# Kernel tuning notes

Hardware: AMD Instinct MI355X
Metric: run time of the kernel (lower is better)

The kernel has to match this reference:

```python
import jax, jax.numpy as jnp
import numpy as np

H = 16          # nhead
N_LAYERS = 4    # stacks (weights are SHARED across stacks, as in the torch module)
PAD_IDX = 1
EPS = 1e-6
NEG = -1e9


def _pos_encoding(S, d):
    den = jnp.exp(-jnp.arange(0, d, 2, dtype=jnp.float32) * (np.log(10000.0) / d))
    ang = jnp.arange(S, dtype=jnp.float32)[:, None] * den[None, :]  # (S, d/2)
    pe = jnp.zeros((S, d), jnp.float32)
    pe = pe.at[:, 0::2].set(jnp.sin(ang)).at[:, 1::2].set(jnp.cos(ang))
    return pe


def _layer_norm(x, g, b):
    mu = jnp.mean(x, axis=-1, keepdims=True)
    var = jnp.mean((x - mu) ** 2, axis=-1, keepdims=True)
    return (x - mu) * jax.lax.rsqrt(var + EPS) * g + b


def _split_heads(x):
    B, S, d = x.shape
    return x.reshape(B, S, H, d // H).transpose(0, 2, 1, 3)  # (B,H,S,dk)


def _mha(q_in, k_in, v_in, mask, wq, bq, wk, bk, wv, bv, wo, bo):
    q = _split_heads(q_in @ wq + bq)
    k = _split_heads(k_in @ wk + bk)
    v = _split_heads(v_in @ wv + bv)
    dk = v.shape[-1]
    score = jnp.einsum('bhqd,bhkd->bhqk', q, k) / jnp.sqrt(jnp.float32(dk))
    if mask is not None:
        score = jnp.where(mask, score, NEG)
    p = jax.nn.softmax(score, axis=-1)
    out = jnp.einsum('bhqk,bhkd->bhqd', p, v)
    B, _, S, _ = out.shape
    out = out.transpose(0, 2, 1, 3).reshape(B, S, H * dk)
    return out @ wo + bo


def setup_inputs() -> dict:
    key = jax.random.key(0)
    B, St, Sm, d, dff, V = 4, 1024, 1024, 1024, 4096, 32000
    ks = jax.random.split(key, 32)
    sc = 1.0 / np.sqrt(d)
    inp = {
        'target_result': jax.random.randint(ks[0], (B, St), 0, V),
        'memory': jax.random.normal(ks[1], (B, Sm, d), jnp.float32),
        'emb': jax.random.normal(ks[2], (V, d), jnp.float32) * sc,
        'ff_w1': jax.random.normal(ks[3], (d, dff), jnp.float32) * sc,
        'ff_b1': jnp.zeros((dff,), jnp.float32),
        'ff_w2': jax.random.normal(ks[4], (dff, d), jnp.float32) / np.sqrt(dff),
        'ff_b2': jnp.zeros((d,), jnp.float32),
        'ln_g': jnp.ones((d,), jnp.float32),
        'ln_b': jnp.zeros((d,), jnp.float32),
    }
    i = 5
    for pre in ('sa', 'xa'):
        for nm in ('q', 'k', 'v', 'o'):
            inp[f'{pre}_w{nm}'] = jax.random.normal(ks[i], (d, d), jnp.float32) * sc
            inp[f'{pre}_b{nm}'] = jnp.zeros((d,), jnp.float32)
            i += 1
    return inp


def reference(target_result, memory, emb,
              sa_wq, sa_bq, sa_wk, sa_bk, sa_wv, sa_bv, sa_wo, sa_bo,
              xa_wq, xa_bq, xa_wk, xa_bk, xa_wv, xa_bv, xa_wo, xa_bo,
              ff_w1, ff_b1, ff_w2, ff_b2, ln_g, ln_b):
    B, St = target_result.shape
    d = emb.shape[1]
    # embed + scale + positional encoding (dropout = eval/identity)
    x = emb[target_result] * jnp.sqrt(jnp.float32(d)) + _pos_encoding(St, d)[None]
    # masks: pad mask (B,1,St,1) & causal (St,St) -> (B,1,St,St); source mask all-ones -> None
    pad = (target_result != PAD_IDX)[:, None, :, None]
    causal = jnp.tril(jnp.ones((St, St), bool))[None, None]
    tgt_mask = pad & causal
    out = x
    for _ in range(N_LAYERS):
        n = _layer_norm(out, ln_g, ln_b)
        out = out + _mha(n, n, n, tgt_mask,
                         sa_wq, sa_bq, sa_wk, sa_bk, sa_wv, sa_bv, sa_wo, sa_bo)
        n = _layer_norm(out, ln_g, ln_b)
        out = out + _mha(n, memory, memory, None,
                         xa_wq, xa_bq, xa_wk, xa_bk, xa_wv, xa_bv, xa_wo, xa_bo)
        n = _layer_norm(out, ln_g, ln_b)
        out = out + (jax.nn.relu(n @ ff_w1 + ff_b1) @ ff_w2 + ff_b2)
    return _layer_norm(out, ln_g, ln_b)
```

## Files before the change

### kernel.cpp

```cpp
#include <hip/hip_runtime.h>

typedef unsigned short u16;
typedef unsigned int u32;
typedef float f32x4 __attribute__((ext_vector_type(4)));
typedef float f32x16 __attribute__((ext_vector_type(16)));
typedef __bf16 bf16x8 __attribute__((ext_vector_type(8)));
typedef short short8 __attribute__((ext_vector_type(8)));
typedef u32 u32x4 __attribute__((ext_vector_type(4)));

#define DINLINE static __device__ __forceinline__

DINLINE u16 f2bf(float f) {
  u32 u = __builtin_bit_cast(u32, f);
  u += 0x7fffu + ((u >> 16) & 1u);
  return (u16)(u >> 16);
}

DINLINE float b2f(u32 lo16) {
  u32 u = lo16 << 16;
  return __builtin_bit_cast(float, u);
}

DINLINE f32x4 mfma16(short8 a, short8 b, f32x4 c) {
  return __builtin_amdgcn_mfma_f32_16x16x32_bf16(
      __builtin_bit_cast(bf16x8, a), __builtin_bit_cast(bf16x8, b), c, 0, 0, 0);
}

DINLINE f32x16 mfma32(short8 a, short8 b, f32x16 c) {
  return __builtin_amdgcn_mfma_f32_32x32x16_bf16(
      __builtin_bit_cast(bf16x8, a), __builtin_bit_cast(bf16x8, b), c, 0, 0, 0);
}

DINLINE u32 cvtpk(float lo, float hi) {
  u32 r;
  asm("v_cvt_pk_bf16_f32 %0, %1, %2" : "=v"(r) : "v"(lo), "v"(hi));
  return r;
}

DINLINE void plswap(u32& a, u32& b) {
  auto r = __builtin_amdgcn_permlane32_swap(a, b, false, false);
  a = (u32)r[0];
  b = (u32)r[1];
}

DINLINE void gld16(const void* g, void* l) {
  __builtin_amdgcn_global_load_lds(
      (const __attribute__((address_space(1))) void*)g,
      (__attribute__((address_space(3))) void*)l, 16, 0, 0);
}

__global__ __launch_bounds__(256) void transpose_wt(const float* __restrict__ src,
                                                    u16* __restrict__ dst, int K, int N,
                                                    float scale) {
  __shared__ float tile[32][33];
  int n0 = blockIdx.x * 32, k0 = blockIdx.y * 32;
  int tx = threadIdx.x, ty = threadIdx.y;
#pragma unroll
  for (int j = 0; j < 32; j += 8)
    tile[ty + j][tx] = src[(size_t)(k0 + ty + j) * N + n0 + tx];
  __syncthreads();
#pragma unroll
  for (int j = 0; j < 32; j += 8)
    dst[(size_t)(n0 + ty + j) * K + k0 + tx] = f2bf(tile[tx][ty + j] * scale);
}

__global__ __launch_bounds__(256) void cvt_bf16(const float* __restrict__ src,
                                                u16* __restrict__ dst) {
  size_t i = (size_t)blockIdx.x * 256 + threadIdx.x;
  float4 v = ((const float4*)src)[i];
  u32 lo = (u32)f2bf(v.x) | ((u32)f2bf(v.y) << 16);
  u32 hi = (u32)f2bf(v.z) | ((u32)f2bf(v.w) << 16);
  uint2 o; o.x = lo; o.y = hi;
  ((uint2*)dst)[i] = o;
}

__global__ void concat3(const float* __restrict__ a, const float* __restrict__ b,
                        const float* __restrict__ c, float* __restrict__ o, float sa) {
  int i = blockIdx.x * 256 + threadIdx.x;
  float v = (i < 1024) ? a[i] * sa : (i < 2048 ? b[i - 1024] : c[i - 2048]);
  o[i] = v;
}

__global__ void scale_vec(const float* __restrict__ a, float* __restrict__ o, float s) {
  int i = blockIdx.x * 256 + threadIdx.x;
  o[i] = a[i] * s;
}

__global__ __launch_bounds__(256) void pe_k(float* __restrict__ pe) {
  int s = blockIdx.x;
  for (int c = threadIdx.x; c < 1024; c += 256) {
    int i = c >> 1;
    float den = expf(-(float)(2 * i) * 0.0089944739960705f);
    float ang = (float)s * den;
    pe[s * 1024 + c] = (c & 1) ? cosf(ang) : sinf(ang);
  }
}

__global__ __launch_bounds__(256) void embed_pe(const int* __restrict__ tgt,
                                                const float* __restrict__ emb,
                                                const float* __restrict__ pe,
                                                float* __restrict__ x,
                                                u16* __restrict__ xbf) {
  int row = blockIdx.x;
  int s = row & 1023;
  int tok = tgt[row];
  float4 e = ((const float4*)(emb + (size_t)tok * 1024))[threadIdx.x];
  float4 p = ((const float4*)(pe + (size_t)s * 1024))[threadIdx.x];
  float4 o;
  o.x = e.x * 32.0f + p.x; o.y = e.y * 32.0f + p.y;
  o.z = e.z * 32.0f + p.z; o.w = e.w * 32.0f + p.w;
  ((float4*)(x + (size_t)row * 1024))[threadIdx.x] = o;
  ushort4 ob;
  ob.x = f2bf(o.x); ob.y = f2bf(o.y); ob.z = f2bf(o.z); ob.w = f2bf(o.w);
  ((ushort4*)(xbf + (size_t)row * 1024))[threadIdx.x] = ob;
}

template <int MODE>
__global__ __launch_bounds__(256) void ln2_k(const float* __restrict__ Xf,
                                             const u16* __restrict__ Xb,
                                             const float* __restrict__ g,
                                             const float* __restrict__ bta,
                                             u16* __restrict__ obf,
                                             float* __restrict__ of) {
  const int t = threadIdx.x;
  const int row = blockIdx.x * 2 + (t >> 7);
  const int c = t & 127;
  float v[8];
  if (MODE == 1) {
    float4 a = ((const float4*)(Xf + (size_t)row * 1024))[c * 2];
    float4 b4 = ((const float4*)(Xf + (size_t)row * 1024))[c * 2 + 1];
    v[0] = a.x; v[1] = a.y; v[2] = a.z; v[3] = a.w;
    v[4] = b4.x; v[5] = b4.y; v[6] = b4.z; v[7] = b4.w;
  } else {
    u32x4 p = *(const u32x4*)(Xb + (size_t)row * 1024 + c * 8);
#pragma unroll
    for (int i = 0; i < 4; ++i) {
      v[2 * i] = b2f(p[i]);
      v[2 * i + 1] = b2f(p[i] >> 16);
    }
  }
  float s = 0.f, sq = 0.f;
#pragma unroll
  for (int i = 0; i < 8; ++i) { s += v[i]; sq += v[i] * v[i]; }
#pragma unroll
  for (int o = 1; o < 64; o <<= 1) {
    s += __shfl_xor(s, o);
    sq += __shfl_xor(sq, o);
  }
  __shared__ float red[8];
  const int wid = t >> 6;
  if ((t & 63) == 0) { red[wid * 2] = s; red[wid * 2 + 1] = sq; }
  __syncthreads();
  const int base = (t >> 7) * 4;
  s = red[base] + red[base + 2];
  sq = red[base + 1] + red[base + 3];
  float mean = s * (1.0f / 1024.0f);
  float var = sq * (1.0f / 1024.0f) - mean * mean;
  float rstd = rsqrtf(var + 1e-6f);
  float4 g0 = ((const float4*)g)[c * 2], g1 = ((const float4*)g)[c * 2 + 1];
  float4 b0 = ((const float4*)bta)[c * 2], b1 = ((const float4*)bta)[c * 2 + 1];
  float gv[8] = {g0.x, g0.y, g0.z, g0.w, g1.x, g1.y, g1.z, g1.w};
  float bv[8] = {b0.x, b0.y, b0.z, b0.w, b1.x, b1.y, b1.z, b1.w};
  float y[8];
#pragma unroll
  for (int i = 0; i < 8; ++i) y[i] = (v[i] - mean) * rstd * gv[i] + bv[i];
  if (MODE == 1) {
    float4 o0, o1;
    o0.x = y[0]; o0.y = y[1]; o0.z = y[2]; o0.w = y[3];
    o1.x = y[4]; o1.y = y[5]; o1.z = y[6]; o1.w = y[7];
    ((float4*)(of + (size_t)row * 1024))[c * 2] = o0;
    ((float4*)(of + (size_t)row * 1024))[c * 2 + 1] = o1;
  } else {
    u32x4 o;
#pragma unroll
    for (int i = 0; i < 4; ++i)
      o[i] = (u32)f2bf(y[2 * i]) | ((u32)f2bf(y[2 * i + 1]) << 16);
    *(u32x4*)(obf + (size_t)row * 1024 + c * 8) = o;
  }
}

template <int BM, int EPI>
__global__ __launch_bounds__(256) void gemm2(
    const u16* __restrict__ A, const u16* __restrict__ Bt,
    const float* __restrict__ bias, float* __restrict__ X,
    u16* __restrict__ Cbf, int N, int K) {
  constexpr int ABYT = BM * 128;
  constexpr int BBYT = 128 * 128;
  constexpr int MF = BM / 32;
  __shared__ __align__(16) char smem[2 * (ABYT + BBYT)];

  const int tid = threadIdx.x;
  const int w = tid >> 6, l = tid & 63;
  const int lg = l >> 4, lc = l & 15;
  const int nwg = gridDim.x * gridDim.y;
  int bid = blockIdx.y * gridDim.x + blockIdx.x;
  bid = (bid & 7) * (nwg >> 3) + (bid >> 3);
  const int m0 = (bid / gridDim.x) * BM, n0 = (bid % gridDim.x) * 128;
  const int wr = w >> 1, wc = w & 1;
  const char* Ab = (const char*)A;
  const char* Bb = (const char*)Bt;
  const size_t sA = (size_t)K * 2;

  f32x4 acc[MF][4];
  const f32x4 zv = {0.f, 0.f, 0.f, 0.f};
#pragma unroll
  for (int m = 0; m < MF; ++m)
#pragma unroll
    for (int n = 0; n < 4; ++n) acc[m][n] = zv;

  const int srow = l >> 3;
  const int scol = ((l & 7) ^ srow) << 4;

  auto stage = [&](char* bufA, char* bufB, int kt) {
    const size_t kb = (size_t)kt << 7;
#pragma unroll
    for (int i = 0; i < BM / 32; ++i) {
      const int r = i * 32 + w * 8 + srow;
      gld16(Ab + (size_t)(m0 + r) * sA + kb + scol, bufA + (i * 4 + w) * 1024 + l * 16);
    }
#pragma unroll
    for (int i = 0; i < 4; ++i) {
      const int r = i * 32 + w * 8 + srow;
      gld16(Bb + (size_t)(n0 + r) * sA + kb + scol, bufB + (i * 4 + w) * 1024 + l * 16);
    }
  };

  stage(smem, smem + ABYT, 0);
  __syncthreads();

  const int nkt = K >> 6;
  int cur = 0;
  for (int kt = 0; kt < nkt; ++kt) {
    char* As = smem + cur * (ABYT + BBYT);
    char* Bs = As + ABYT;
    if (kt + 1 < nkt) {
      char* An = smem + (cur ^ 1) * (ABYT + BBYT);
      stage(An, An + ABYT, kt + 1);
    }
    __builtin_amdgcn_s_setprio(1);
#pragma unroll
    for (int ks = 0; ks < 2; ++ks) {
      short8 af[MF], bf4[4];
#pragma unroll
      for (int m = 0; m < MF; ++m) {
        int row = wr * (BM / 2) + m * 16 + lc;
        int col = (ks * 64 + (lg << 4)) ^ ((row & 7) << 4);
        af[m] = *(const short8*)(As + row * 128 + col);
      }
#pragma unroll
      for (int n = 0; n < 4; ++n) {
        int row = wc * 64 + n * 16 + lc;
        int col = (ks * 64 + (lg << 4)) ^ ((row & 7) << 4);
        bf4[n] = *(const short8*)(Bs + row * 128 + col);
      }
#pragma unroll
      for (int m = 0; m < MF; ++m)
#pragma unroll
        for (int n = 0; n < 4; ++n) acc[m][n] = mfma16(af[m], bf4[n], acc[m][n]);
    }
    __builtin_amdgcn_s_setprio(0);
    __syncthreads();
    cur ^= 1;
  }

  float bv[4];
#pragma unroll
  for (int n = 0; n < 4; ++n) bv[n] = bias[n0 + wc * 64 + n * 16 + lc];

  if (EPI <= 1) {
    u16* ct = (u16*)smem;
#pragma unroll
    for (int m = 0; m < MF; ++m)
#pragma unroll
      for (int n = 0; n < 4; ++n)
#pragma unroll
        for (int r = 0; r < 4; ++r) {
          int row = wr * (BM / 2) + m * 16 + (lg << 2) + r;
          int col = wc * 64 + n * 16 + lc;
          float v = acc[m][n][r] + bv[n];
          if (EPI == 1) v = v > 0.f ? v : 0.f;
          ct[row * 136 + col] = f2bf(v);
        }
    __syncthreads();
#pragma unroll
    for (int j = 0; j < BM / 16; ++j) {
      int c = j * 256 + tid;
      int row = c >> 4, colb = (c & 15) * 8;
      *(short8*)(Cbf + (size_t)(m0 + row) * N + n0 + colb) =
          *(const short8*)(ct + row * 136 + colb);
    }
  } else if (EPI == 2) {
    float* cf = (float*)smem;
#pragma unroll
    for (int m = 0; m < MF; ++m)
#pragma unroll
      for (int n = 0; n < 4; ++n)
#pragma unroll
        for (int r = 0; r < 4; ++r) {
          int row = wr * (BM / 2) + m * 16 + (lg << 2) + r;
          int col = wc * 64 + n * 16 + lc;
          cf[row * 128 + col] = acc[m][n][r] + bv[n];
        }
    __syncthreads();
#pragma unroll
    for (int j = 0; j < BM / 8; ++j) {
      int c = j * 256 + tid;
      int row = c >> 5, colb = (c & 31) * 4;
      size_t idx = (size_t)(m0 + row) * N + n0 + colb;
      float4 s4 = *(const float4*)(cf + row * 128 + colb);
      float4 xv = *(const float4*)(X + idx);
      xv.x += s4.x; xv.y += s4.y; xv.z += s4.z; xv.w += s4.w;
      *(float4*)(X + idx) = xv;
      ushort4 ob;
      ob.x = f2bf(xv.x); ob.y = f2bf(xv.y); ob.z = f2bf(xv.z); ob.w = f2bf(xv.w);
      *(ushort4*)(Cbf + idx) = ob;
    }
  } else {
    u16* ct = (u16*)smem;
#pragma unroll
    for (int m = 0; m < MF; ++m)
#pragma unroll
      for (int n = 0; n < 4; ++n)
#pragma unroll
        for (int r = 0; r < 4; ++r) {
          int row = wr * (BM / 2) + m * 16 + (lg << 2) + r;
          int col = wc * 64 + n * 16 + lc;
          ct[col * 136 + row] = f2bf(acc[m][n][r] + bv[n]);
        }
    __syncthreads();
    const int bb = m0 >> 10, ms = m0 & 1023;
#pragma unroll
    for (int j = 0; j < BM / 16; ++j) {
      int flat = j * 256 + tid;
      int sb = flat & (BM / 8 - 1);
      int col = flat / (BM / 8);
      int n = n0 + col;
      u16* dst = Cbf + (size_t)(((bb << 4) + (n >> 6)) * 64 + (n & 63)) * 1024 + ms + sb * 8;
      *(short8*)dst = *(const short8*)(ct + col * 136 + sb * 8);
    }
  }
}

template <int BM, int EPI>
__global__ __launch_bounds__(256) void gemm2c(
    const u16* __restrict__ A, const u16* __restrict__ Bt,
    const float* __restrict__ bias, float* __restrict__ X,
    u16* __restrict__ Cbf, int N, int K) {
  constexpr int ABYT = BM * 128;
  constexpr int BBYT = 128 * 128;
  constexpr int BUF = ABYT + BBYT;
  constexpr int MF = BM / 32;
  __shared__ __align__(16) char smem[3 * BUF];

  const int tid = threadIdx.x;
  const int w = tid >> 6, l = tid & 63;
  const int lg = l >> 4, lc = l & 15;
  const int nwg = gridDim.x * gridDim.y;
  int bid = blockIdx.y * gridDim.x + blockIdx.x;
  bid = (bid & 7) * (nwg >> 3) + (bid >> 3);
  const int m0 = (bid / gridDim.x) * BM, n0 = (bid % gridDim.x) * 128;
  const int wr = w >> 1, wc = w & 1;
  const char* Ab = (const char*)A;
  const char* Bb = (const char*)Bt;
  const size_t sA = (size_t)K * 2;

  f32x4 acc[MF][4];
  const f32x4 zv = {0.f, 0.f, 0.f, 0.f};
#pragma unroll
  for (int m = 0; m < MF; ++m)
#pragma unroll
    for (int n = 0; n < 4; ++n) acc[m][n] = zv;

  const int srow = l >> 3;
  const int scol = ((l & 7) ^ srow) << 4;

  auto stage = [&](char* buf, int kt) {
    const size_t kb = (size_t)kt << 7;
#pragma unroll
    for (int i = 0; i < BM / 32; ++i) {
      const int r = i * 32 + w * 8 + srow;
      gld16(Ab + (size_t)(m0 + r) * sA + kb + scol, buf + (i * 4 + w) * 1024 + l * 16);
    }
#pragma unroll
    for (int i = 0; i < 4; ++i) {
      const int r = i * 32 + w * 8 + srow;
      gld16(Bb + (size_t)(n0 + r) * sA + kb + scol,
            buf + ABYT + (i * 4 + w) * 1024 + l * 16);
    }
  };

  char* p0 = smem;
  char* p1 = smem + BUF;
  char* p2 = smem + 2 * BUF;

  stage(p0, 0);
  stage(p1, 1);
  __builtin_amdgcn_sched_barrier(0);
  asm volatile("s_waitcnt vmcnt(6)" ::: "memory");
  __builtin_amdgcn_s_barrier();
  __builtin_amdgcn_sched_barrier(0);

  const int nkt = K >> 6;
  for (int kt = 0; kt < nkt; ++kt) {
    if (kt + 2 < nkt) stage(p2, kt + 2);
    const char* As = p0;
    const char* Bs = p0 + ABYT;
    __builtin_amdgcn_s_setprio(1);
#pragma unroll
    for (int ks = 0; ks < 2; ++ks) {
      short8 af[MF], bf4[4];
#pragma unroll
      for (int m = 0; m < MF; ++m) {
        int row = wr * (BM / 2) + m * 16 + lc;
        int col = (ks * 64 + (lg << 4)) ^ ((row & 7) << 4);
        af[m] = *(const short8*)(As + row * 128 + col);
      }
#pragma unroll
      for (int n = 0; n < 4; ++n) {
        int row = wc * 64 + n * 16 + lc;
        int col = (ks * 64 + (lg << 4)) ^ ((row & 7) << 4);
        bf4[n] = *(const short8*)(Bs + row * 128 + col);
      }
#pragma unroll
      for (int m = 0; m < MF; ++m)
#pragma unroll
        for (int n = 0; n < 4; ++n) acc[m][n] = mfma16(af[m], bf4[n], acc[m][n]);
    }
    __builtin_amdgcn_s_setprio(0);
    __builtin_amdgcn_sched_barrier(0);
    if (kt + 2 < nkt) {
      asm volatile("s_waitcnt vmcnt(6) lgkmcnt(0)" ::: "memory");
    } else {
      asm volatile("s_waitcnt vmcnt(0) lgkmcnt(0)" ::: "memory");
    }
    __builtin_amdgcn_s_barrier();
    __builtin_amdgcn_sched_barrier(0);
    char* t = p0; p0 = p1; p1 = p2; p2 = t;
  }

  float bv[4];
#pragma unroll
  for (int n = 0; n < 4; ++n) bv[n] = bias[n0 + wc * 64 + n * 16 + lc];

  if (EPI <= 1) {
    u16* ct = (u16*)smem;
#pragma unroll
    for (int m = 0; m < MF; ++m)
#pragma unroll
      for (int n = 0; n < 4; ++n)
#pragma unroll
        for (int r = 0; r < 4; ++r) {
          int row = wr * (BM / 2) + m * 16 + (lg << 2) + r;
          int col = wc * 64 + n * 16 + lc;
          float v = acc[m][n][r] + bv[n];
          if (EPI == 1) v = v > 0.f ? v : 0.f;
          ct[row * 136 + col] = f2bf(v);
        }
    __syncthreads();
#pragma unroll
    for (int j = 0; j < BM / 16; ++j) {
      int c = j * 256 + tid;
      int row = c >> 4, colb = (c & 15) * 8;
      *(short8*)(Cbf + (size_t)(m0 + row) * N + n0 + colb) =
          *(const short8*)(ct + row * 136 + colb);
    }
  } else if (EPI == 2) {
    float* cf = (float*)smem;
#pragma unroll
    for (int m = 0; m < MF; ++m)
#pragma unroll
      for (int n = 0; n < 4; ++n)
#pragma unroll
        for (int r = 0; r < 4; ++r) {
          int row = wr * (BM / 2) + m * 16 + (lg << 2) + r;
          int col = wc * 64 + n * 16 + lc;
          cf[row * 128 + col] = acc[m][n][r] + bv[n];
        }
    __syncthreads();
#pragma unroll
    for (int j = 0; j < BM / 8; ++j) {
      int c = j * 256 + tid;
      int row = c >> 5, colb = (c & 31) * 4;
      size_t idx = (size_t)(m0 + row) * N + n0 + colb;
      float4 s4 = *(const float4*)(cf + row * 128 + colb);
      float4 xv = *(const float4*)(X + idx);
      xv.x += s4.x; xv.y += s4.y; xv.z += s4.z; xv.w += s4.w;
      *(float4*)(X + idx) = xv;
      ushort4 ob;
      ob.x = f2bf(xv.x); ob.y = f2bf(xv.y); ob.z = f2bf(xv.z); ob.w = f2bf(xv.w);
      *(ushort4*)(Cbf + idx) = ob;
    }
  } else {
    u16* ct = (u16*)smem;
#pragma unroll
    for (int m = 0; m < MF; ++m)
#pragma unroll
      for (int n = 0; n < 4; ++n)
#pragma unroll
        for (int r = 0; r < 4; ++r) {
          int row = wr * (BM / 2) + m * 16 + (lg << 2) + r;
          int col = wc * 64 + n * 16 + lc;
          ct[col * 136 + row] = f2bf(acc[m][n][r] + bv[n]);
        }
    __syncthreads();
    const int bb = m0 >> 10, ms = m0 & 1023;
#pragma unroll
    for (int j = 0; j < BM / 16; ++j) {
      int flat = j * 256 + tid;
      int sb = flat & (BM / 8 - 1);
      int col = flat / (BM / 8);
      int n = n0 + col;
      u16* dst = Cbf + (size_t)(((bb << 4) + (n >> 6)) * 64 + (n & 63)) * 1024 + ms + sb * 8;
      *(short8*)dst = *(const short8*)(ct + col * 136 + sb * 8);
    }
  }
}

template <int EPI>
__global__ __launch_bounds__(512) void gemm3b(
    const u16* __restrict__ A, const u16* __restrict__ Bt,
    const float* __restrict__ bias, u16* __restrict__ Cbf, int N, int K) {
  constexpr int ABYT = 32768;
  constexpr int BBYT = 32768;
  __shared__ __align__(16) char smem[2 * (ABYT + BBYT)];

  const int tid = threadIdx.x;
  const int w = tid >> 6, l = tid & 63;
  const int lg = l >> 4, lc = l & 15;
  const int nwg = gridDim.x * gridDim.y;
  int bid = blockIdx.y * gridDim.x + blockIdx.x;
  bid = (bid & 7) * (nwg >> 3) + (bid >> 3);
  const int m0 = (bid / gridDim.x) * 256, n0 = (bid % gridDim.x) * 256;
  const int wr = w >> 2, wc = w & 3;
  const char* Ab = (const char*)A;
  const char* Bb = (const char*)Bt;
  const size_t sA = (size_t)K * 2;

  f32x4 acc[8][4];
  const f32x4 zv = {0.f, 0.f, 0.f, 0.f};
#pragma unroll
  for (int m = 0; m < 8; ++m)
#pragma unroll
    for (int n = 0; n < 4; ++n) acc[m][n] = zv;

  const int srow = l >> 3;
  const int scol = ((l & 7) ^ srow) << 4;

  auto stage = [&](char* buf, int kt) {
    const size_t kb = (size_t)kt << 7;
#pragma unroll
    for (int i = 0; i < 4; ++i) {
      const int r = i * 64 + w * 8 + srow;
      gld16(Ab + (size_t)(m0 + r) * sA + kb + scol, buf + (i * 8 + w) * 1024 + l * 16);
    }
#pragma unroll
    for (int i = 0; i < 4; ++i) {
      const int r = i * 64 + w * 8 + srow;
      gld16(Bb + (size_t)(n0 + r) * sA + kb + scol,
            buf + ABYT + (i * 8 + w) * 1024 + l * 16);
    }
  };

  stage(smem, 0);
  __syncthreads();

  const int nkt = K >> 6;
  int cur = 0;
  for (int kt = 0; kt < nkt; ++kt) {
    char* As = smem + cur * (ABYT + BBYT);
    char* Bs = As + ABYT;
    if (kt + 1 < nkt) stage(smem + (cur ^ 1) * (ABYT + BBYT), kt + 1);
    __builtin_amdgcn_s_setprio(1);
#pragma unroll
    for (int ks = 0; ks < 2; ++ks) {
      short8 bf4[4];
#pragma unroll
      for (int n = 0; n < 4; ++n) {
        int row = wc * 64 + n * 16 + lc;
        int col = (ks * 64 + (lg << 4)) ^ ((row & 7) << 4);
        bf4[n] = *(const short8*)(Bs + row * 128 + col);
      }
#pragma unroll
      for (int m = 0; m < 8; ++m) {
        int row = wr * 128 + m * 16 + lc;
        int col = (ks * 64 + (lg << 4)) ^ ((row & 7) << 4);
        short8 af = *(const short8*)(As + row * 128 + col);
#pragma unroll
        for (int n = 0; n < 4; ++n) acc[m][n] = mfma16(af, bf4[n], acc[m][n]);
      }
    }
    __builtin_amdgcn_s_setprio(0);
    __syncthreads();
    cur ^= 1;
  }

  float bv[4];
#pragma unroll
  for (int n = 0; n < 4; ++n) bv[n] = bias[n0 + wc * 64 + n * 16 + lc];
  u16* ct = (u16*)smem;
#pragma unroll
  for (int h = 0; h < 2; ++h) {
    __syncthreads();
    if (wr == h) {
#pragma unroll
      for (int m = 0; m < 8; ++m)
#pragma unroll
        for (int n = 0; n < 4; ++n)
#pragma unroll
          for (int r = 0; r < 4; ++r) {
            int row = m * 16 + (lg << 2) + r;
            int col = wc * 64 + n * 16 + lc;
            float v = acc[m][n][r] + bv[n];
            if (EPI == 1) v = v > 0.f ? v : 0.f;
            ct[row * 264 + col] = f2bf(v);
          }
    }
    __syncthreads();
#pragma unroll
    for (int j = 0; j < 8; ++j) {
      int c = j * 512 + tid;
      int row = c >> 5, colb = (c & 31) * 8;
      *(short8*)(Cbf + (size_t)(m0 + h * 128 + row) * N + n0 + colb) =
          *(const short8*)(ct + row * 264 + colb);
    }
  }
}

template <bool CAUSAL>
__global__ __launch_bounds__(512) void attn_lds(
    const u16* __restrict__ Qp, int sQ, const u16* __restrict__ Kp, int sK,
    const u16* __restrict__ Vt, const int* __restrict__ tgt,
    u16* __restrict__ Out) {
  __shared__ __align__(16) char smem[2][32768];
  const int tid = threadIdx.x;
  const int w = tid >> 6, l = tid & 63;
  const int bh = blockIdx.x & 63;
  const int p = blockIdx.x >> 6;
  const int qt = CAUSAL ? ((w < 4) ? (p * 4 + w) : (31 - (p * 4 + (w - 4))))
                        : (p * 8 + w);
  const int b = bh >> 4, h = bh & 15;
  const int lq = l & 31, hi = l >> 5;
  const int q0 = qt * 32;

  const char* Kc = (const char*)(Kp + (size_t)b * 1024 * sK + h * 64);
  const char* Vc = (const char*)(Vt + (size_t)bh * 64 * 1024);
  const u16* Qh = Qp + (size_t)b * 1024 * sQ + h * 64;

  short8 qb[4];
  {
    const u16* qrow = Qh + (size_t)(q0 + lq) * sQ + hi * 8;
#pragma unroll
    for (int c = 0; c < 4; ++c) qb[c] = *(const short8*)(qrow + c * 16);
  }

  bool row_ok = true;
  int my_nkt = 16;
  int blk_nst = CAUSAL ? (8 - p) : 8;
  if (CAUSAL) {
    row_ok = (tgt[b * 1024 + q0 + lq] != 1);
    bool anypad_w = __any(!row_ok);
    __shared__ int s_pad;
    if (tid == 0) s_pad = 0;
    __syncthreads();
    if (anypad_w && l == 0) s_pad = 1;
    __syncthreads();
    if (s_pad) { my_nkt = 16; blk_nst = 8; }
    else my_nkt = (qt >> 1) + 1;
  }

  const int srow = l >> 3;
  const int scol = ((l & 7) ^ srow) << 4;
  auto stage = [&](int buf, int st) {
    const int k0 = st * 128;
    char* Ks = smem[buf];
    char* Vs = smem[buf] + 16384;
    const int r = w * 8 + srow;
#pragma unroll
    for (int t2 = 0; t2 < 2; ++t2) {
      gld16(Kc + (size_t)(k0 + t2 * 64 + r) * sK * 2 + scol, Ks + t2 * 8192 + r * 128);
      gld16(Vc + (size_t)r * 2048 + (size_t)(k0 + t2 * 64) * 2 + scol,
            Vs + t2 * 8192 + r * 128);
    }
  };

  float m = -3.0e38f, lsum = 0.f;
  f32x16 oacc[2];
#pragma unroll
  for (int r = 0; r < 16; ++r) { oacc[0][r] = 0.f; oacc[1][r] = 0.f; }

  stage(0, 0);
  __syncthreads();
  int cur = 0;

  for (int st = 0; st < blk_nst; ++st) {
    if (st + 1 < blk_nst) stage(cur ^ 1, st + 1);
#pragma unroll
    for (int t2 = 0; t2 < 2; ++t2) {
      const int t64 = st * 2 + t2;
      if (t64 < my_nkt) {
        const char* Ks = smem[cur] + t2 * 8192;
        const char* Vs = smem[cur] + 16384 + t2 * 8192;
        const int k0 = t64 * 64;
        f32x16 stt[2];
        __builtin_amdgcn_s_setprio(1);
#pragma unroll
        for (int s = 0; s < 2; ++s) {
          const int row = s * 32 + lq;
          const int swz = (row & 7) << 4;
          f32x16 a;
#pragma unroll
          for (int r = 0; r < 16; ++r) a[r] = 0.f;
#pragma unroll
          for (int c = 0; c < 4; ++c) {
            short8 kb = *(const short8*)(Ks + row * 128 + ((c * 32 + hi * 16) ^ swz));
            a = mfma32(kb, qb[c], a);
          }
          stt[s] = a;
        }
        __builtin_amdgcn_s_setprio(0);
        if (CAUSAL) {
#pragma unroll
          for (int s = 0; s < 2; ++s) {
            if (!row_ok || (k0 + s * 32 + 31 > q0)) {
#pragma unroll
              for (int r = 0; r < 16; ++r) {
                int kg = k0 + s * 32 + (r & 3) + 8 * (r >> 2) + 4 * hi;
                bool ok = row_ok && (kg <= q0 + lq);
                if (!ok) stt[s][r] = -1e9f;
              }
            }
          }
        }
        float tm;
        {
          float v[16];
#pragma unroll
          for (int r = 0; r < 16; ++r) v[r] = fmaxf(stt[0][r], stt[1][r]);
#pragma unroll
          for (int w2 = 8; w2 >= 1; w2 >>= 1)
#pragma unroll
            for (int r = 0; r < w2; ++r) v[r] = fmaxf(v[r], v[r + w2]);
          tm = v[0];
        }
        tm = fmaxf(tm, __shfl_xor(tm, 32));
        if (!__all(tm <= m + 8.0f)) {
          float mn = fmaxf(m, tm);
          float alpha = __expf(m - mn);
          lsum *= alpha;
          m = mn;
#pragma unroll
          for (int r = 0; r < 16; ++r) {
            int crow = (r & 3) + 8 * (r >> 2) + 4 * hi;
            float av = __shfl(alpha, crow);
            oacc[0][r] *= av;
            oacc[1][r] *= av;
          }
        }
        float tsa0 = 0.f, tsa1 = 0.f, tsa2 = 0.f, tsa3 = 0.f;
#pragma unroll
        for (int s = 0; s < 2; ++s) {
#pragma unroll
          for (int r = 0; r < 16; ++r) {
            float e = __expf(stt[s][r] - m);
            stt[s][r] = e;
            if ((r & 3) == 0) tsa0 += e;
            else if ((r & 3) == 1) tsa1 += e;
            else if ((r & 3) == 2) tsa2 += e;
            else tsa3 += e;
          }
        }
        float ts = (tsa0 + tsa1) + (tsa2 + tsa3);
        ts += __shfl_xor(ts, 32);
        lsum += ts;
        short8 pa[4];
#pragma unroll
        for (int s = 0; s < 2; ++s) {
          u32 cc[8];
#pragma unroll
          for (int t = 0; t < 4; ++t) {
            cc[2 * t]     = cvtpk(stt[s][4 * t + 0], stt[s][4 * t + 1]);
            cc[2 * t + 1] = cvtpk(stt[s][4 * t + 2], stt[s][4 * t + 3]);
          }
          plswap(cc[0], cc[2]);
          plswap(cc[1], cc[3]);
          plswap(cc[4], cc[6]);
          plswap(cc[5], cc[7]);
          u32x4 w0 = {cc[0], cc[1], cc[2], cc[3]};
          u32x4 w1 = {cc[4], cc[5], cc[6], cc[7]};
          pa[2 * s]     = __builtin_bit_cast(short8, w0);
          pa[2 * s + 1] = __builtin_bit_cast(short8, w1);
        }
        __builtin_amdgcn_s_setprio(1);
#pragma unroll
        for (int dt = 0; dt < 2; ++dt) {
          const int row = dt * 32 + lq;
          const int swz = (row & 7) << 4;
#pragma unroll
          for (int c = 0; c < 4; ++c) {
            short8 vb = *(const short8*)(Vs + row * 128 + ((c * 32 + hi * 16) ^ swz));
            oacc[dt] = mfma32(pa[c], vb, oacc[dt]);
          }
        }
        __builtin_amdgcn_s_setprio(0);
      }
    }
    __syncthreads();
    cur ^= 1;
  }

#pragma unroll
  for (int r = 0; r < 16; ++r) {
    int crow = (r & 3) + 8 * (r >> 2) + 4 * hi;
    float lv = __shfl(lsum, crow);
    float linv = 1.0f / lv;
    int qg = q0 + crow;
    size_t base = ((size_t)b * 1024 + qg) * 1024 + h * 64 + lq;
    Out[base] = f2bf(oacc[0][r] * linv);
    Out[base + 32] = f2bf(oacc[1][r] * linv);
  }
}

extern "C" void kernel_launch(void* const* d_in, const int* in_sizes, int n_in,
                              void* d_out, int out_size, void* d_ws, size_t ws_size,
                              hipStream_t stream) {
  const int* tgt = (const int*)d_in[0];
  const float* memory = (const float*)d_in[1];
  const float* emb = (const float*)d_in[2];
  const float* ff_w1 = (const float*)d_in[3];
  const float* ff_b1 = (const float*)d_in[4];
  const float* ff_w2 = (const float*)d_in[5];
  const float* ff_b2 = (const float*)d_in[6];
  const float* ln_g = (const float*)d_in[7];
  const float* ln_b = (const float*)d_in[8];
  const float* sa_wq = (const float*)d_in[9];
  const float* sa_bq = (const float*)d_in[10];
  const float* sa_wk = (const float*)d_in[11];
  const float* sa_bk = (const float*)d_in[12];
  const float* sa_wv = (const float*)d_in[13];
  const float* sa_bv = (const float*)d_in[14];
  const float* sa_wo = (const float*)d_in[15];
  const float* sa_bo = (const float*)d_in[16];
  const float* xa_wq = (const float*)d_in[17];
  const float* xa_bq = (const float*)d_in[18];
  const float* xa_wk = (const float*)d_in[19];
  const float* xa_bk = (const float*)d_in[20];
  const float* xa_wv = (const float*)d_in[21];
  const float* xa_bv = (const float*)d_in[22];
  const float* xa_wo = (const float*)d_in[23];
  const float* xa_bo = (const float*)d_in[24];

  char* ws = (char*)d_ws;
  size_t off = 0;
  auto alloc = [&](size_t bytes) {
    char* p = ws + off;
    off += (bytes + 255) & ~(size_t)255;
    return p;
  };
  float* x   = (float*)alloc(4096ull * 1024 * 4);
  u16* xbf   = (u16*)alloc(4096ull * 1024 * 2);
  u16* nbf   = (u16*)alloc(4096ull * 1024 * 2);
  u16* qkv   = (u16*)alloc(4096ull * 2048 * 2);
  u16* q2    = (u16*)alloc(4096ull * 1024 * 2);
  u16* attn  = (u16*)alloc(4096ull * 1024 * 2);
  u16* vt    = (u16*)alloc(64ull * 64 * 1024 * 2);
  u16* kx    = (u16*)alloc(4096ull * 1024 * 2);
  u16* vtx   = (u16*)alloc(64ull * 64 * 1024 * 2);
  u16* h1    = (u16*)alloc(4096ull * 4096 * 2);
  u16* memb  = (u16*)alloc(4096ull * 1024 * 2);
  u16* w_qkv = (u16*)alloc(3072ull * 1024 * 2);
  u16* w_sao = (u16*)alloc(1024ull * 1024 * 2);
  u16* w_xaq = (u16*)alloc(1024ull * 1024 * 2);
  u16* w_xak = (u16*)alloc(1024ull * 1024 * 2);
  u16* w_xav = (u16*)alloc(1024ull * 1024 * 2);
  u16* w_xao = (u16*)alloc(1024ull * 1024 * 2);
  u16* w_ff1 = (u16*)alloc(4096ull * 1024 * 2);
  u16* w_ff2 = (u16*)alloc(1024ull * 4096 * 2);
  float* b_qkv = (float*)alloc(3072 * 4);
  float* b_xaq = (float*)alloc(1024 * 4);
  float* pe    = (float*)alloc(1024ull * 1024 * 4);

  dim3 blk(256);
  dim3 b32(32, 8);
  const float QS = 0.125f;

  transpose_wt<<<dim3(32, 32), b32, 0, stream>>>(sa_wq, w_qkv, 1024, 1024, QS);
  transpose_wt<<<dim3(32, 32), b32, 0, stream>>>(sa_wk, w_qkv + 1024 * 1024, 1024, 1024, 1.f);
  transpose_wt<<<dim3(32, 32), b32, 0, stream>>>(sa_wv, w_qkv + 2048 * 1024, 1024, 1024, 1.f);
  transpose_wt<<<dim3(32, 32), b32, 0, stream>>>(sa_wo, w_sao, 1024, 1024, 1.f);
  transpose_wt<<<dim3(32, 32), b32, 0, stream>>>(xa_wq, w_xaq, 1024, 1024, QS);
  transpose_wt<<<dim3(32, 32), b32, 0, stream>>>(xa_wk, w_xak, 1024, 1024, 1.f);
  transpose_wt<<<dim3(32, 32), b32, 0, stream>>>(xa_wv, w_xav, 1024, 1024, 1.f);
  transpose_wt<<<dim3(32, 32), b32, 0, stream>>>(xa_wo, w_xao, 1024, 1024, 1.f);
  transpose_wt<<<dim3(128, 32), b32, 0, stream>>>(ff_w1, w_ff1, 1024, 4096, 1.f);
  transpose_wt<<<dim3(32, 128), b32, 0, stream>>>(ff_w2, w_ff2, 4096, 1024, 1.f);
  concat3<<<12, blk, 0, stream>>>(sa_bq, sa_bk, sa_bv, b_qkv, QS);
  scale_vec<<<4, blk, 0, stream>>>(xa_bq, b_xaq, QS);
  cvt_bf16<<<4096, blk, 0, stream>>>(memory, memb);
  pe_k<<<1024, blk, 0, stream>>>(pe);
  embed_pe<<<4096, blk, 0, stream>>>(tgt, emb, pe, x, xbf);

  gemm2c<64, 0><<<dim3(8, 64), blk, 0, stream>>>(memb, w_xak, xa_bk, nullptr, kx, 1024, 1024);
  gemm2c<64, 3><<<dim3(8, 64), blk, 0, stream>>>(memb, w_xav, xa_bv, nullptr, vtx, 1024, 1024);

  for (int layer = 0; layer < 4; ++layer) {
    ln2_k<2><<<2048, blk, 0, stream>>>(nullptr, xbf, ln_g, ln_b, nbf, nullptr);
    gemm2<128, 0><<<dim3(16, 32), blk, 0, stream>>>(nbf, w_qkv, b_qkv, nullptr, qkv, 2048, 1024);
    gemm2c<64, 3><<<dim3(8, 64), blk, 0, stream>>>(nbf, w_qkv + 2048 * 1024, b_qkv + 2048,
                                                   nullptr, vt, 1024, 1024);
    attn_lds<true><<<256, dim3(512), 0, stream>>>(qkv, 2048, qkv + 1024, 2048, vt, tgt, attn);
    gemm2c<64, 2><<<dim3(8, 64), blk, 0, stream>>>(attn, w_sao, sa_bo, x, xbf, 1024, 1024);
    ln2_k<2><<<2048, blk, 0, stream>>>(nullptr, xbf, ln_g, ln_b, nbf, nullptr);
    gemm2c<64, 0><<<dim3(8, 64), blk, 0, stream>>>(nbf, w_xaq, b_xaq, nullptr, q2, 1024, 1024);
    attn_lds<false><<<256, dim3(512), 0, stream>>>(q2, 1024, kx, 1024, vtx, nullptr, attn);
    gemm2c<64, 2><<<dim3(8, 64), blk, 0, stream>>>(attn, w_xao, xa_bo, x, xbf, 1024, 1024);
    ln2_k<2><<<2048, blk, 0, stream>>>(nullptr, xbf, ln_g, ln_b, nbf, nullptr);
    gemm3b<1><<<dim3(16, 16), dim3(512), 0, stream>>>(nbf, w_ff1, ff_b1, h1, 4096, 1024);
    gemm2c<64, 2><<<dim3(8, 64), blk, 0, stream>>>(h1, w_ff2, ff_b2, x, xbf, 1024, 4096);
  }
  ln2_k<1><<<2048, blk, 0, stream>>>(x, nullptr, ln_g, ln_b, nullptr, (float*)d_out);
}
```

Before: 1.045 ms.

## Fuse self-attention QKV projections into one 256x256-tile GEMM with split epilogue

Replaces the separate Q/K GEMM and V-transposed GEMM with a single gemm3q kernel. It uses 256x256 tiles and 512 threads, and its epilogue writes Q/K row-major or V transposed depending on the column range. The aim is to remove one launch, reuse the A operand across all three projections, and raise per-block arithmetic intensity. The grid is 192 blocks, fewer than the CU count, so occupancy may suffer. The old gemm2 kernel is removed and its code is renamed to become gemm2c.

```diff
diff --git a/kernel.cpp b/kernel.cpp
--- a/kernel.cpp
+++ b/kernel.cpp
@@ -180,14 +180,15 @@
 }
 
 template <int BM, int EPI>
-__global__ __launch_bounds__(256) void gemm2(
+__global__ __launch_bounds__(256) void gemm2c(
     const u16* __restrict__ A, const u16* __restrict__ Bt,
     const float* __restrict__ bias, float* __restrict__ X,
     u16* __restrict__ Cbf, int N, int K) {
   constexpr int ABYT = BM * 128;
   constexpr int BBYT = 128 * 128;
+  constexpr int BUF = ABYT + BBYT;
   constexpr int MF = BM / 32;
-  __shared__ __align__(16) char smem[2 * (ABYT + BBYT)];
+  __shared__ __align__(16) char smem[3 * BUF];
 
   const int tid = threadIdx.x;
   const int w = tid >> 6, l = tid & 63;
@@ -211,32 +212,37 @@
   const int srow = l >> 3;
   const int scol = ((l & 7) ^ srow) << 4;
 
-  auto stage = [&](char* bufA, char* bufB, int kt) {
+  auto stage = [&](char* buf, int kt) {
     const size_t kb = (size_t)kt << 7;
 #pragma unroll
     for (int i = 0; i < BM / 32; ++i) {
       const int r = i * 32 + w * 8 + srow;
-      gld16(Ab + (size_t)(m0 + r) * sA + kb + scol, bufA + (i * 4 + w) * 1024 + l * 16);
+      gld16(Ab + (size_t)(m0 + r) * sA + kb + scol, buf + (i * 4 + w) * 1024 + l * 16);
     }
 #pragma unroll
     for (int i = 0; i < 4; ++i) {
       const int r = i * 32 + w * 8 + srow;
-      gld16(Bb + (size_t)(n0 + r) * sA + kb + scol, bufB + (i * 4 + w) * 1024 + l * 16);
+      gld16(Bb + (size_t)(n0 + r) * sA + kb + scol,
+            buf + ABYT + (i * 4 + w) * 1024 + l * 16);
     }
   };
 
-  stage(smem, smem + ABYT, 0);
-  __syncthreads();
+  char* p0 = smem;
+  char* p1 = smem + BUF;
+  char* p2 = smem + 2 * BUF;
+
+  stage(p0, 0);
+  stage(p1, 1);
+  __builtin_amdgcn_sched_barrier(0);
+  asm volatile("s_waitcnt vmcnt(6)" ::: "memory");
+  __builtin_amdgcn_s_barrier();
+  __builtin_amdgcn_sched_barrier(0);
 
   const int nkt = K >> 6;
-  int cur = 0;
   for (int kt = 0; kt < nkt; ++kt) {
-    char* As = smem + cur * (ABYT + BBYT);
-    char* Bs = As + ABYT;
-    if (kt + 1 < nkt) {
-      char* An = smem + (cur ^ 1) * (ABYT + BBYT);
-      stage(An, An + ABYT, kt + 1);
-    }
+    if (kt + 2 < nkt) stage(p2, kt + 2);
+    const char* As = p0;
+    const char* Bs = p0 + ABYT;
     __builtin_amdgcn_s_setprio(1);
 #pragma unroll
     for (int ks = 0; ks < 2; ++ks) {
@@ -259,8 +265,15 @@
         for (int n = 0; n < 4; ++n) acc[m][n] = mfma16(af[m], bf4[n], acc[m][n]);
     }
     __builtin_amdgcn_s_setprio(0);
-    __syncthreads();
-    cur ^= 1;
+    __builtin_amdgcn_sched_barrier(0);
+    if (kt + 2 < nkt) {
+      asm volatile("s_waitcnt vmcnt(6) lgkmcnt(0)" ::: "memory");
+    } else {
+      asm volatile("s_waitcnt vmcnt(0) lgkmcnt(0)" ::: "memory");
+    }
+    __builtin_amdgcn_s_barrier();
+    __builtin_amdgcn_sched_barrier(0);
+    char* t = p0; p0 = p1; p1 = p2; p2 = t;
   }
 
   float bv[4];
@@ -341,181 +354,6 @@
   }
 }
 
-template <int BM, int EPI>
-__global__ __launch_bounds__(256) void gemm2c(
-    const u16* __restrict__ A, const u16* __restrict__ Bt,
-    const float* __restrict__ bias, float* __restrict__ X,
-    u16* __restrict__ Cbf, int N, int K) {
-  constexpr int ABYT = BM * 128;
-  constexpr int BBYT = 128 * 128;
-  constexpr int BUF = ABYT + BBYT;
-  constexpr int MF = BM / 32;
-  __shared__ __align__(16) char smem[3 * BUF];
-
-  const int tid = threadIdx.x;
-  const int w = tid >> 6, l = tid & 63;
-  const int lg = l >> 4, lc = l & 15;
-  const int nwg = gridDim.x * gridDim.y;
-  int bid = blockIdx.y * gridDim.x + blockIdx.x;
-  bid = (bid & 7) * (nwg >> 3) + (bid >> 3);
-  const int m0 = (bid / gridDim.x) * BM, n0 = (bid % gridDim.x) * 128;
-  const int wr = w >> 1, wc = w & 1;
-  const char* Ab = (const char*)A;
-  const char* Bb = (const char*)Bt;
-  const size_t sA = (size_t)K * 2;
-
-  f32x4 acc[MF][4];
-  const f32x4 zv = {0.f, 0.f, 0.f, 0.f};
-#pragma unroll
-  for (int m = 0; m < MF; ++m)
-#pragma unroll
-    for (int n = 0; n < 4; ++n) acc[m][n] = zv;
-
-  const int srow = l >> 3;
-  const int scol = ((l & 7) ^ srow) << 4;
-
-  auto stage = [&](char* buf, int kt) {
-    const size_t kb = (size_t)kt << 7;
-#pragma unroll
-    for (int i = 0; i < BM / 32; ++i) {
-      const int r = i * 32 + w * 8 + srow;
-      gld16(Ab + (size_t)(m0 + r) * sA + kb + scol, buf + (i * 4 + w) * 1024 + l * 16);
-    }
-#pragma unroll
-    for (int i = 0; i < 4; ++i) {
-      const int r = i * 32 + w * 8 + srow;
-      gld16(Bb + (size_t)(n0 + r) * sA + kb + scol,
-            buf + ABYT + (i * 4 + w) * 1024 + l * 16);
-    }
-  };
-
-  char* p0 = smem;
-  char* p1 = smem + BUF;
-  char* p2 = smem + 2 * BUF;
-
-  stage(p0, 0);
-  stage(p1, 1);
-  __builtin_amdgcn_sched_barrier(0);
-  asm volatile("s_waitcnt vmcnt(6)" ::: "memory");
-  __builtin_amdgcn_s_barrier();
-  __builtin_amdgcn_sched_barrier(0);
-
-  const int nkt = K >> 6;
-  for (int kt = 0; kt < nkt; ++kt) {
-    if (kt + 2 < nkt) stage(p2, kt + 2);
-    const char* As = p0;
-    const char* Bs = p0 + ABYT;
-    __builtin_amdgcn_s_setprio(1);
-#pragma unroll
-    for (int ks = 0; ks < 2; ++ks) {
-      short8 af[MF], bf4[4];
-#pragma unroll
-      for (int m = 0; m < MF; ++m) {
-        int row = wr * (BM / 2) + m * 16 + lc;
-        int col = (ks * 64 + (lg << 4)) ^ ((row & 7) << 4);
-        af[m] = *(const short8*)(As + row * 128 + col);
-      }
-#pragma unroll
-      for (int n = 0; n < 4; ++n) {
-        int row = wc * 64 + n * 16 + lc;
-        int col = (ks * 64 + (lg << 4)) ^ ((row & 7) << 4);
-        bf4[n] = *(const short8*)(Bs + row * 128 + col);
-      }
-#pragma unroll
-      for (int m = 0; m < MF; ++m)
-#pragma unroll
-        for (int n = 0; n < 4; ++n) acc[m][n] = mfma16(af[m], bf4[n], acc[m][n]);
-    }
-    __builtin_amdgcn_s_setprio(0);
-    __builtin_amdgcn_sched_barrier(0);
-    if (kt + 2 < nkt) {
-      asm volatile("s_waitcnt vmcnt(6) lgkmcnt(0)" ::: "memory");
-    } else {
-      asm volatile("s_waitcnt vmcnt(0) lgkmcnt(0)" ::: "memory");
-    }
-    __builtin_amdgcn_s_barrier();
-    __builtin_amdgcn_sched_barrier(0);
-    char* t = p0; p0 = p1; p1 = p2; p2 = t;
-  }
-
-  float bv[4];
-#pragma unroll
-  for (int n = 0; n < 4; ++n) bv[n] = bias[n0 + wc * 64 + n * 16 + lc];
-
-  if (EPI <= 1) {
-    u16* ct = (u16*)smem;
-#pragma unroll
-    for (int m = 0; m < MF; ++m)
-#pragma unroll
-      for (int n = 0; n < 4; ++n)
-#pragma unroll
-        for (int r = 0; r < 4; ++r) {
-          int row = wr * (BM / 2) + m * 16 + (lg << 2) + r;
-          int col = wc * 64 + n * 16 + lc;
-          float v = acc[m][n][r] + bv[n];
-          if (EPI == 1) v = v > 0.f ? v : 0.f;
-          ct[row * 136 + col] = f2bf(v);
-        }
-    __syncthreads();
-#pragma unroll
-    for (int j = 0; j < BM / 16; ++j) {
-      int c = j * 256 + tid;
-      int row = c >> 4, colb = (c & 15) * 8;
-      *(short8*)(Cbf + (size_t)(m0 + row) * N + n0 + colb) =
-          *(const short8*)(ct + row * 136 + colb);
-    }
-  } else if (EPI == 2) {
-    float* cf = (float*)smem;
-#pragma unroll
-    for (int m = 0; m < MF; ++m)
-#pragma unroll
-      for (int n = 0; n < 4; ++n)
-#pragma unroll
-        for (int r = 0; r < 4; ++r) {
-          int row = wr * (BM / 2) + m * 16 + (lg << 2) + r;
-          int col = wc * 64 + n * 16 + lc;
-          cf[row * 128 + col] = acc[m][n][r] + bv[n];
-        }
-    __syncthreads();
-#pragma unroll
-    for (int j = 0; j < BM / 8; ++j) {
-      int c = j * 256 + tid;
-      int row = c >> 5, colb = (c & 31) * 4;
-      size_t idx = (size_t)(m0 + row) * N + n0 + colb;
-      float4 s4 = *(const float4*)(cf + row * 128 + colb);
-      float4 xv = *(const float4*)(X + idx);
-      xv.x += s4.x; xv.y += s4.y; xv.z += s4.z; xv.w += s4.w;
-      *(float4*)(X + idx) = xv;
-      ushort4 ob;
-      ob.x = f2bf(xv.x); ob.y = f2bf(xv.y); ob.z = f2bf(xv.z); ob.w = f2bf(xv.w);
-      *(ushort4*)(Cbf + idx) = ob;
-    }
-  } else {
-    u16* ct = (u16*)smem;
-#pragma unroll
-    for (int m = 0; m < MF; ++m)
-#pragma unroll
-      for (int n = 0; n < 4; ++n)
-#pragma unroll
-        for (int r = 0; r < 4; ++r) {
-          int row = wr * (BM / 2) + m * 16 + (lg << 2) + r;
-          int col = wc * 64 + n * 16 + lc;
-          ct[col * 136 + row] = f2bf(acc[m][n][r] + bv[n]);
-        }
-    __syncthreads();
-    const int bb = m0 >> 10, ms = m0 & 1023;
-#pragma unroll
-    for (int j = 0; j < BM / 16; ++j) {
-      int flat = j * 256 + tid;
-      int sb = flat & (BM / 8 - 1);
-      int col = flat / (BM / 8);
-      int n = n0 + col;
-      u16* dst = Cbf + (size_t)(((bb << 4) + (n >> 6)) * 64 + (n & 63)) * 1024 + ms + sb * 8;
-      *(short8*)dst = *(const short8*)(ct + col * 136 + sb * 8);
-    }
-  }
-}
-
 template <int EPI>
 __global__ __launch_bounds__(512) void gemm3b(
     const u16* __restrict__ A, const u16* __restrict__ Bt,
@@ -622,6 +460,144 @@
       int row = c >> 5, colb = (c & 31) * 8;
       *(short8*)(Cbf + (size_t)(m0 + h * 128 + row) * N + n0 + colb) =
           *(const short8*)(ct + row * 264 + colb);
+    }
+  }
+}
+
+__global__ __launch_bounds__(512) void gemm3q(
+    const u16* __restrict__ A, const u16* __restrict__ Bt,
+    const float* __restrict__ bias, u16* __restrict__ Cqk, u16* __restrict__ Vt, int K) {
+  constexpr int ABYT = 32768;
+  constexpr int BBYT = 32768;
+  __shared__ __align__(16) char smem[2 * (ABYT + BBYT)];
+
+  const int tid = threadIdx.x;
+  const int w = tid >> 6, l = tid & 63;
+  const int lg = l >> 4, lc = l & 15;
+  const int nwg = gridDim.x * gridDim.y;
+  int bid = blockIdx.y * gridDim.x + blockIdx.x;
+  bid = (bid & 7) * (nwg >> 3) + (bid >> 3);
+  const int m0 = (bid / gridDim.x) * 256, n0 = (bid % gridDim.x) * 256;
+  const int wr = w >> 2, wc = w & 3;
+  const char* Ab = (const char*)A;
+  const char* Bb = (const char*)Bt;
+  const size_t sA = (size_t)K * 2;
+
+  f32x4 acc[8][4];
+  const f32x4 zv = {0.f, 0.f, 0.f, 0.f};
+#pragma unroll
+  for (int m = 0; m < 8; ++m)
+#pragma unroll
+    for (int n = 0; n < 4; ++n) acc[m][n] = zv;
+
+  const int srow = l >> 3;
+  const int scol = ((l & 7) ^ srow) << 4;
+
+  auto stage = [&](char* buf, int kt) {
+    const size_t kb = (size_t)kt << 7;
+#pragma unroll
+    for (int i = 0; i < 4; ++i) {
+      const int r = i * 64 + w * 8 + srow;
+      gld16(Ab + (size_t)(m0 + r) * sA + kb + scol, buf + (i * 8 + w) * 1024 + l * 16);
+    }
+#pragma unroll
+    for (int i = 0; i < 4; ++i) {
+      const int r = i * 64 + w * 8 + srow;
+      gld16(Bb + (size_t)(n0 + r) * sA + kb + scol,
+            buf + ABYT + (i * 8 + w) * 1024 + l * 16);
+    }
+  };
+
+  stage(smem, 0);
+  __syncthreads();
+
+  const int nkt = K >> 6;
+  int cur = 0;
+  for (int kt = 0; kt < nkt; ++kt) {
+    char* As = smem + cur * (ABYT + BBYT);
+    char* Bs = As + ABYT;
+    if (kt + 1 < nkt) stage(smem + (cur ^ 1) * (ABYT + BBYT), kt + 1);
+    __builtin_amdgcn_s_setprio(1);
+#pragma unroll
+    for (int ks = 0; ks < 2; ++ks) {
+      short8 bf4[4];
+#pragma unroll
+      for (int n = 0; n < 4; ++n) {
+        int row = wc * 64 + n * 16 + lc;
+        int col = (ks * 64 + (lg << 4)) ^ ((row & 7) << 4);
+        bf4[n] = *(const short8*)(Bs + row * 128 + col);
+      }
+#pragma unroll
+      for (int m = 0; m < 8; ++m) {
+        int row = wr * 128 + m * 16 + lc;
+        int col = (ks * 64 + (lg << 4)) ^ ((row & 7) << 4);
+        short8 af = *(const short8*)(As + row * 128 + col);
+#pragma unroll
+        for (int n = 0; n < 4; ++n) acc[m][n] = mfma16(af, bf4[n], acc[m][n]);
+      }
+    }
+    __builtin_amdgcn_s_setprio(0);
+    __syncthreads();
+    cur ^= 1;
+  }
+
+  float bv[4];
+#pragma unroll
+  for (int n = 0; n < 4; ++n) bv[n] = bias[n0 + wc * 64 + n * 16 + lc];
+  u16* ct = (u16*)smem;
+
+  if (n0 < 2048) {
+#pragma unroll
+    for (int h = 0; h < 2; ++h) {
+      __syncthreads();
+      if (wr == h) {
+#pragma unroll
+        for (int m = 0; m < 8; ++m)
+#pragma unroll
+          for (int n = 0; n < 4; ++n)
+#pragma unroll
+            for (int r = 0; r < 4; ++r) {
+              int row = m * 16 + (lg << 2) + r;
+              int col = wc * 64 + n * 16 + lc;
+              ct[row * 264 + col] = f2bf(acc[m][n][r] + bv[n]);
+            }
+      }
+      __syncthreads();
+#pragma unroll
+      for (int j = 0; j < 8; ++j) {
+        int c = j * 512 + tid;
+        int row = c >> 5, colb = (c & 31) * 8;
+        *(short8*)(Cqk + (size_t)(m0 + h * 128 + row) * 2048 + n0 + colb) =
+            *(const short8*)(ct + row * 264 + colb);
+      }
+    }
+  } else {
+    const int bb = m0 >> 10, ms = m0 & 1023;
+#pragma unroll
+    for (int h = 0; h < 2; ++h) {
+      __syncthreads();
+      if (wr == h) {
+#pragma unroll
+        for (int m = 0; m < 8; ++m)
+#pragma unroll
+          for (int n = 0; n < 4; ++n)
+#pragma unroll
+            for (int r = 0; r < 4; ++r) {
+              int row = m * 16 + (lg << 2) + r;
+              int col = wc * 64 + n * 16 + lc;
+              ct[col * 136 + row] = f2bf(acc[m][n][r] + bv[n]);
+            }
+      }
+      __syncthreads();
+#pragma unroll
+      for (int j = 0; j < 8; ++j) {
+        int flat = j * 512 + tid;
+        int col = flat >> 4, sb = flat & 15;
+        int n = n0 + col - 2048;
+        u16* dst = Vt + (size_t)(((bb << 4) + (n >> 6)) * 64 + (n & 63)) * 1024 +
+                   ms + h * 128 + sb * 8;
+        *(short8*)dst = *(const short8*)(ct + col * 136 + sb * 8);
+      }
     }
   }
 }
@@ -904,9 +880,7 @@
 
   for (int layer = 0; layer < 4; ++layer) {
     ln2_k<2><<<2048, blk, 0, stream>>>(nullptr, xbf, ln_g, ln_b, nbf, nullptr);
-    gemm2<128, 0><<<dim3(16, 32), blk, 0, stream>>>(nbf, w_qkv, b_qkv, nullptr, qkv, 2048, 1024);
-    gemm2c<64, 3><<<dim3(8, 64), blk, 0, stream>>>(nbf, w_qkv + 2048 * 1024, b_qkv + 2048,
-                                                   nullptr, vt, 1024, 1024);
+    gemm3q<<<dim3(12, 16), dim3(512), 0, stream>>>(nbf, w_qkv, b_qkv, qkv, vt, 1024);
     attn_lds<true><<<256, dim3(512), 0, stream>>>(qkv, 2048, qkv + 1024, 2048, vt, tgt, attn);
     gemm2c<64, 2><<<dim3(8, 64), blk, 0, stream>>>(attn, w_sao, sa_bo, x, xbf, 1024, 1024);
     ln2_k<2><<<2048, blk, 0, stream>>>(nullptr, xbf, ln_g, ln_b, nbf, nullptr);
```

New measurement: 1.048 ms. Within noise of the previous version (+0.2%).
